# Optimization experiments

Hardware: AMD Instinct MI355X
Metric: run time of the kernel (lower is better)

## Reference

```python
import jax, jax.numpy as jnp
import numpy as np
from jax import lax

B_SZ, L, D_MODEL = 2, 2048, 1024
D_INNER, D_STATE, D_CONV, DT_RANK = 2048, 16, 4, 64


def setup_inputs() -> dict:
    key = jax.random.key(0)
    ks = jax.random.split(key, 9)
    s = 0.02
    x = jax.random.normal(ks[0], (B_SZ, L, D_MODEL), dtype=jnp.float32)
    W_in = jax.random.normal(ks[1], (D_MODEL, 2 * D_INNER), dtype=jnp.float32) * s
    conv_w = jax.random.normal(ks[2], (D_INNER, D_CONV), dtype=jnp.float32) * s
    conv_b = jax.random.normal(ks[3], (D_INNER,), dtype=jnp.float32) * s
    W_x = jax.random.normal(ks[4], (D_INNER, DT_RANK + 2 * D_STATE), dtype=jnp.float32) * s
    W_dt = jax.random.normal(ks[5], (DT_RANK, D_INNER), dtype=jnp.float32) * s
    b_dt = jax.random.normal(ks[6], (D_INNER,), dtype=jnp.float32) * s
    A_log = jnp.log(jnp.broadcast_to(jnp.arange(1, D_STATE + 1, dtype=jnp.float32), (D_INNER, D_STATE)))
    D = jnp.ones((D_INNER,), dtype=jnp.float32)
    W_out = jax.random.normal(ks[7], (D_INNER, D_MODEL), dtype=jnp.float32) * s
    return {"x": x, "W_in": W_in, "conv_w": conv_w, "conv_b": conv_b,
            "W_x": W_x, "W_dt": W_dt, "b_dt": b_dt, "A_log": A_log, "D": D, "W_out": W_out}


def _silu(v):
    return v * jax.nn.sigmoid(v)


def _mamba_fwd(x, W_in, conv_w, conv_b, W_x, W_dt, b_dt, A_log, D, W_out):
    b, l, _ = x.shape
    xz = x @ W_in                                  # [b,l,2*d_inner]
    xs, res = jnp.split(xz, 2, axis=-1)
    # causal depthwise conv1d (torch pads d_conv-1 both sides then truncates to l -> left pad only)
    xc = xs.transpose(0, 2, 1)                     # [b,d_inner,l]
    xc = lax.conv_general_dilated(
        xc, conv_w[:, None, :], window_strides=(1,),
        padding=[(D_CONV - 1, 0)], feature_group_count=D_INNER,
        dimension_numbers=("NCH", "OIH", "NCH")) + conv_b[None, :, None]
    u = _silu(xc.transpose(0, 2, 1))               # [b,l,d_inner]
    # projections for delta, B, C
    x_dbl = u @ W_x                                # [b,l,dt_rank+2n]
    dt, Bm, Cm = jnp.split(x_dbl, [DT_RANK, DT_RANK + D_STATE], axis=-1)
    delta = jax.nn.softplus(dt @ W_dt + b_dt)      # [b,l,d_inner]
    A = -jnp.exp(A_log)                            # [d_inner,n]

    def step(h, inp):
        d_t, B_t, C_t, u_t = inp                   # [b,d_in],[b,n],[b,n],[b,d_in]
        dA = jnp.exp(d_t[:, :, None] * A)          # [b,d_in,n]
        h = dA * h + d_t[:, :, None] * B_t[:, None, :] * u_t[:, :, None]
        y = jnp.einsum("bdn,bn->bd", h, C_t)
        return h, y

    h0 = jnp.zeros((b, D_INNER, D_STATE), dtype=u.dtype)
    _, ys = lax.scan(step, h0, (delta.transpose(1, 0, 2), Bm.transpose(1, 0, 2),
                                Cm.transpose(1, 0, 2), u.transpose(1, 0, 2)))
    y = ys.transpose(1, 0, 2) + u * D              # [b,l,d_inner]
    y = y * _silu(res)
    return y @ W_out                               # [b,l,d_model]


def reference(x, W_in, conv_w, conv_b, W_x, W_dt, b_dt, A_log, D, W_out):
    return _mamba_fwd(x, W_in, conv_w, conv_b, W_x, W_dt, b_dt, A_log, D, W_out)
```

## Files before the change

### kernel.cpp

```cpp
#include <hip/hip_runtime.h>
#include <hip/hip_bf16.h>
#include <math.h>

#define B_SZ    2
#define LSEQ    2048
#define DMODEL  1024
#define DINNER  2048
#define DSTATE  16
#define DCONV   4
#define DTRANK  64

#define NCHUNK  64
#define CLEN    (LSEQ / NCHUNK)

#define KSPLIT  16
#define NX      96

typedef unsigned short u16;
typedef __bf16 bf16x8 __attribute__((ext_vector_type(8)));
typedef float  f32x4  __attribute__((ext_vector_type(4)));

static __device__ __forceinline__ float sigmoidf_(float x) {
    return 1.0f / (1.0f + __expf(-x));
}
static __device__ __forceinline__ u16 f2b(float f) {
    unsigned int u = __float_as_uint(f);
    u = (u + 0x7fffu + ((u >> 16) & 1u)) >> 16;
    return (u16)u;
}
static __device__ __forceinline__ float b2f(u16 v) {
    return __uint_as_float(((unsigned int)v) << 16);
}

__global__ __launch_bounds__(256) void cast_bf16(
    const float* __restrict__ in, u16* __restrict__ out, int n8)
{
    const int i = blockIdx.x * 256 + threadIdx.x;
    if (i >= n8) return;
    const float4* p = reinterpret_cast<const float4*>(in + (size_t)i * 8);
    float4 v0 = p[0], v1 = p[1];
    union { u16 u[8]; uint4 q; } r;
    r.u[0] = f2b(v0.x); r.u[1] = f2b(v0.y); r.u[2] = f2b(v0.z); r.u[3] = f2b(v0.w);
    r.u[4] = f2b(v1.x); r.u[5] = f2b(v1.y); r.u[6] = f2b(v1.z); r.u[7] = f2b(v1.w);
    reinterpret_cast<uint4*>(out)[i] = r.q;
}

__global__ __launch_bounds__(256) void castT_bf16(
    const float* __restrict__ in, u16* __restrict__ out, int R, int C)
{
    __shared__ float t[32][33];
    const int r0 = blockIdx.y * 32, c0 = blockIdx.x * 32;
    const int tr = threadIdx.x >> 3;
    const int tc4 = (threadIdx.x & 7) * 4;
    const float4 v = *reinterpret_cast<const float4*>(in + (size_t)(r0 + tr) * C + c0 + tc4);
    t[tr][tc4 + 0] = v.x; t[tr][tc4 + 1] = v.y; t[tr][tc4 + 2] = v.z; t[tr][tc4 + 3] = v.w;
    __syncthreads();
    union { u16 u[4]; uint2 q; } r;
    #pragma unroll
    for (int j = 0; j < 4; j++) r.u[j] = f2b(t[tc4 + j][tr]);
    *reinterpret_cast<uint2*>(out + (size_t)(c0 + tr) * R + r0 + tc4) = r.q;
}

__global__ __launch_bounds__(256) void gemm_bf16_split(
    const u16* __restrict__ A, const u16* __restrict__ Bt,
    u16* __restrict__ xs_bf, u16* __restrict__ zs_bf, int K)
{
    __shared__ u16 As[128 * 32];
    __shared__ u16 Bs[128 * 32];
    const int tid  = threadIdx.x;
    const int lane = tid & 63;
    const int wave = tid >> 6;
    const int wr = wave >> 1, wc = wave & 1;
    const int bm = blockIdx.y * 128, bn = blockIdx.x * 128;
    const int lhi = lane >> 4;
    const int llo = lane & 15;

    f32x4 acc[4][4] = {};

    for (int k0 = 0; k0 < K; k0 += 32) {
        #pragma unroll
        for (int c = 0; c < 2; ++c) {
            const int s   = c * 256 + wave * 64 + lane;
            const int row = s >> 2, seg = s & 3;
            const u16* ga = A  + (size_t)(bm + row) * K + k0 + seg * 8;
            const u16* gb = Bt + (size_t)(bn + row) * K + k0 + seg * 8;
            __builtin_amdgcn_global_load_lds(
                (const __attribute__((address_space(1))) void*)ga,
                (__attribute__((address_space(3))) void*)(As + (size_t)(c * 256 + wave * 64) * 8),
                16, 0, 0);
            __builtin_amdgcn_global_load_lds(
                (const __attribute__((address_space(1))) void*)gb,
                (__attribute__((address_space(3))) void*)(Bs + (size_t)(c * 256 + wave * 64) * 8),
                16, 0, 0);
        }
        __syncthreads();

        bf16x8 af[4], bfr[4];
        #pragma unroll
        for (int m = 0; m < 4; ++m)
            af[m] = *reinterpret_cast<const bf16x8*>(&As[(wr * 64 + m * 16 + llo) * 32 + lhi * 8]);
        #pragma unroll
        for (int n = 0; n < 4; ++n)
            bfr[n] = *reinterpret_cast<const bf16x8*>(&Bs[(wc * 64 + n * 16 + llo) * 32 + lhi * 8]);
        #pragma unroll
        for (int m = 0; m < 4; ++m)
            #pragma unroll
            for (int n = 0; n < 4; ++n)
                acc[m][n] = __builtin_amdgcn_mfma_f32_16x16x32_bf16(af[m], bfr[n], acc[m][n], 0, 0, 0);
        __syncthreads();
    }

    #pragma unroll
    for (int m = 0; m < 4; ++m) {
        const int row0 = bm + wr * 64 + m * 16 + lhi * 4;
        #pragma unroll
        for (int n = 0; n < 4; ++n) {
            const int col = bn + wc * 64 + n * 16 + llo;
            #pragma unroll
            for (int j = 0; j < 4; ++j) {
                float v = acc[m][n][j];
                if (col < DINNER) {
                    xs_bf[(size_t)(row0 + j) * DINNER + col] = f2b(v);
                } else {
                    v = v * sigmoidf_(v);
                    zs_bf[(size_t)(row0 + j) * DINNER + (col - DINNER)] = f2b(v);
                }
            }
        }
    }
}

__global__ __launch_bounds__(256) void gemm_bf16_tn(
    const u16* __restrict__ A, const u16* __restrict__ Bt,
    float* __restrict__ C, int M, int N, int K, int ldc)
{
    __shared__ u16 As[128 * 32];
    __shared__ u16 Bs[128 * 32];
    const int tid  = threadIdx.x;
    const int lane = tid & 63;
    const int wave = tid >> 6;
    const int wr = wave >> 1, wc = wave & 1;
    const int bm = blockIdx.y * 128, bn = blockIdx.x * 128;
    const int lhi = lane >> 4;
    const int llo = lane & 15;

    f32x4 acc[4][4] = {};

    for (int k0 = 0; k0 < K; k0 += 32) {
        #pragma unroll
        for (int c = 0; c < 2; ++c) {
            const int s   = c * 256 + wave * 64 + lane;
            const int row = s >> 2, seg = s & 3;
            const u16* ga = A  + (size_t)(bm + row) * K + k0 + seg * 8;
            const u16* gb = Bt + (size_t)(bn + row) * K + k0 + seg * 8;
            __builtin_amdgcn_global_load_lds(
                (const __attribute__((address_space(1))) void*)ga,
                (__attribute__((address_space(3))) void*)(As + (size_t)(c * 256 + wave * 64) * 8),
                16, 0, 0);
            __builtin_amdgcn_global_load_lds(
                (const __attribute__((address_space(1))) void*)gb,
                (__attribute__((address_space(3))) void*)(Bs + (size_t)(c * 256 + wave * 64) * 8),
                16, 0, 0);
        }
        __syncthreads();

        bf16x8 af[4], bfr[4];
        #pragma unroll
        for (int m = 0; m < 4; ++m)
            af[m] = *reinterpret_cast<const bf16x8*>(&As[(wr * 64 + m * 16 + llo) * 32 + lhi * 8]);
        #pragma unroll
        for (int n = 0; n < 4; ++n)
            bfr[n] = *reinterpret_cast<const bf16x8*>(&Bs[(wc * 64 + n * 16 + llo) * 32 + lhi * 8]);
        #pragma unroll
        for (int m = 0; m < 4; ++m)
            #pragma unroll
            for (int n = 0; n < 4; ++n)
                acc[m][n] = __builtin_amdgcn_mfma_f32_16x16x32_bf16(af[m], bfr[n], acc[m][n], 0, 0, 0);
        __syncthreads();
    }

    #pragma unroll
    for (int m = 0; m < 4; ++m) {
        const int row0 = bm + wr * 64 + m * 16 + lhi * 4;
        #pragma unroll
        for (int n = 0; n < 4; ++n) {
            const int col = bn + wc * 64 + n * 16 + llo;
            #pragma unroll
            for (int j = 0; j < 4; ++j)
                C[(size_t)(row0 + j) * ldc + col] = acc[m][n][j];
        }
    }
}

__global__ __launch_bounds__(256) void conv_silu_bf(
    const u16* __restrict__ xs, const float* __restrict__ conv_w,
    const float* __restrict__ conv_b, u16* __restrict__ u)
{
    const int g  = blockIdx.x * 256 + threadIdx.x;
    const int d8 = (g & 255) * 8;
    const int bl = g >> 8;
    const int l  = bl & (LSEQ - 1);

    float4 wv[8];
    #pragma unroll
    for (int j = 0; j < 8; j++)
        wv[j] = *reinterpret_cast<const float4*>(conv_w + (size_t)(d8 + j) * DCONV);

    float acc[8];
    #pragma unroll
    for (int j = 0; j < 8; j++) acc[j] = conv_b[d8 + j];

    #pragma unroll
    for (int k = 0; k < DCONV; k++) {
        const int l2 = l - (DCONV - 1) + k;
        if (l2 < 0) continue;
        const uint4 q = *reinterpret_cast<const uint4*>(
            xs + (size_t)(bl - (DCONV - 1) + k) * DINNER + d8);
        const u16* e = reinterpret_cast<const u16*>(&q);
        #pragma unroll
        for (int j = 0; j < 8; j++) {
            const float w = (k == 0) ? wv[j].x : (k == 1) ? wv[j].y : (k == 2) ? wv[j].z : wv[j].w;
            acc[j] = fmaf(b2f(e[j]), w, acc[j]);
        }
    }
    union { u16 u[8]; uint4 q; } r;
    #pragma unroll
    for (int j = 0; j < 8; j++) {
        const float v = acc[j];
        r.u[j] = f2b(v * sigmoidf_(v));
    }
    *reinterpret_cast<uint4*>(u + (size_t)bl * DINNER + d8) = r.q;
}

__global__ __launch_bounds__(256) void gemm3_splitk(
    const u16* __restrict__ ubf, const float* __restrict__ Wx,
    float* __restrict__ partial)
{
    __shared__ float us[64][65];
    __shared__ float wsm[64][96];

    const int tid = threadIdx.x;
    const int r0 = blockIdx.x * 64;
    const int k0 = blockIdx.y * (DINNER / KSPLIT);

    const int orow = tid >> 2;
    const int oc0  = (tid & 3) * 24;

    float acc[24];
    #pragma unroll
    for (int j = 0; j < 24; j++) acc[j] = 0.f;

    for (int ks = 0; ks < DINNER / KSPLIT; ks += 64) {
        {
            const int row = tid >> 2;
            const int c16 = (tid & 3) << 4;
            const uint4* src = reinterpret_cast<const uint4*>(
                ubf + (size_t)(r0 + row) * DINNER + k0 + ks + c16);
            const uint4 q0 = src[0], q1 = src[1];
            const u16* e0 = reinterpret_cast<const u16*>(&q0);
            const u16* e1 = reinterpret_cast<const u16*>(&q1);
            #pragma unroll
            for (int j = 0; j < 8; j++) us[row][c16 + j]     = b2f(e0[j]);
            #pragma unroll
            for (int j = 0; j < 8; j++) us[row][c16 + 8 + j] = b2f(e1[j]);
        }
        #pragma unroll
        for (int j = 0; j < 6; j++) {
            const int fid = tid + j * 256;
            const int kr  = fid / 24;
            const int c4  = (fid % 24) * 4;
            *reinterpret_cast<float4*>(&wsm[kr][c4]) =
                *reinterpret_cast<const float4*>(Wx + (size_t)(k0 + ks + kr) * NX + c4);
        }
        __syncthreads();

        for (int kk = 0; kk < 64; ++kk) {
            const float uv = us[orow][kk];
            #pragma unroll
            for (int j = 0; j < 24; j++)
                acc[j] = fmaf(uv, wsm[kk][oc0 + j], acc[j]);
        }
        __syncthreads();
    }

    float* pp = partial + ((size_t)blockIdx.y * (B_SZ * LSEQ) + r0 + orow) * NX + oc0;
    #pragma unroll
    for (int j = 0; j < 24; j += 4)
        *reinterpret_cast<float4*>(pp + j) = make_float4(acc[j], acc[j+1], acc[j+2], acc[j+3]);
}

__global__ __launch_bounds__(256) void gemm3_reduce(
    const float* __restrict__ partial, float* __restrict__ xdbl)
{
    const int i = blockIdx.x * 256 + threadIdx.x;
    if (i >= B_SZ * LSEQ * NX / 4) return;
    float4 s = make_float4(0.f, 0.f, 0.f, 0.f);
    #pragma unroll
    for (int p = 0; p < KSPLIT; p++) {
        const float4 v = reinterpret_cast<const float4*>(
            partial + (size_t)p * (B_SZ * LSEQ) * NX)[i];
        s.x += v.x; s.y += v.y; s.z += v.z; s.w += v.w;
    }
    reinterpret_cast<float4*>(xdbl)[i] = s;
}

__global__ __launch_bounds__(256) void scan_phase1(
    const u16* __restrict__ ubf, const float* __restrict__ xdbl,
    const float* __restrict__ Wdt, const float* __restrict__ bdt,
    const float* __restrict__ A_log,
    float* __restrict__ hend, float* __restrict__ Sd, u16* __restrict__ delta_bf)
{
    const int idx = blockIdx.x * 256 + threadIdx.x;
    const int d = idx & (DINNER - 1);
    const int c = (idx >> 11) & (NCHUNK - 1);
    const int b = idx >> 17;

    float w[DTRANK];
    #pragma unroll
    for (int k = 0; k < DTRANK; k++) w[k] = Wdt[(size_t)k * DINNER + d];
    const float bb = bdt[d];

    float a[DSTATE];
    #pragma unroll
    for (int n = 0; n < DSTATE; n++) a[n] = -__expf(A_log[d * DSTATE + n]);

    float h[DSTATE];
    #pragma unroll
    for (int n = 0; n < DSTATE; n++) h[n] = 0.f;
    float sd = 0.f;

    const int l0 = b * LSEQ + c * CLEN;
    for (int i = 0; i < CLEN; ++i) {
        const size_t r = (size_t)(l0 + i);
        const float* xr = xdbl + r * NX;

        float t = bb;
        #pragma unroll
        for (int k = 0; k < DTRANK; k += 4) {
            const float4 v = *reinterpret_cast<const float4*>(xr + k);
            t = fmaf(w[k],     v.x, t);
            t = fmaf(w[k + 1], v.y, t);
            t = fmaf(w[k + 2], v.z, t);
            t = fmaf(w[k + 3], v.w, t);
        }
        const float dv = (t > 20.f) ? t : log1pf(__expf(t));
        sd += dv;
        delta_bf[r * DINNER + d] = f2b(dv);

        const float uv = b2f(ubf[r * DINNER + d]);

        float Bv[DSTATE];
        {
            const float4* bp = reinterpret_cast<const float4*>(xr + DTRANK);
            float4 q;
            q = bp[0]; Bv[0]=q.x;  Bv[1]=q.y;  Bv[2]=q.z;  Bv[3]=q.w;
            q = bp[1]; Bv[4]=q.x;  Bv[5]=q.y;  Bv[6]=q.z;  Bv[7]=q.w;
            q = bp[2]; Bv[8]=q.x;  Bv[9]=q.y;  Bv[10]=q.z; Bv[11]=q.w;
            q = bp[3]; Bv[12]=q.x; Bv[13]=q.y; Bv[14]=q.z; Bv[15]=q.w;
        }
        const float du = dv * uv;
        #pragma unroll
        for (int n = 0; n < DSTATE; n++)
            h[n] = fmaf(__expf(dv * a[n]), h[n], du * Bv[n]);
    }

    float* hp = hend + ((size_t)(b * DINNER + d) * NCHUNK + c) * DSTATE;
    #pragma unroll
    for (int n = 0; n < DSTATE; n += 4)
        *reinterpret_cast<float4*>(hp + n) = make_float4(h[n], h[n+1], h[n+2], h[n+3]);
    Sd[(size_t)(b * DINNER + d) * NCHUNK + c] = sd;
}

__global__ __launch_bounds__(256) void scan_phase2(
    float* __restrict__ hend, const float* __restrict__ Sd,
    const float* __restrict__ A_log)
{
    const int idx = blockIdx.x * 256 + threadIdx.x;
    if (idx >= B_SZ * DINNER * DSTATE) return;
    const int n = idx & (DSTATE - 1);
    const int d = (idx >> 4) & (DINNER - 1);
    const int b = idx >> 15;

    const float an = -__expf(A_log[d * DSTATE + n]);
    const size_t base = (size_t)(b * DINNER + d) * NCHUNK;
    float carry = 0.f;
    for (int c = 0; c < NCHUNK; ++c) {
        const float P = __expf(an * Sd[base + c]);
        const size_t off = (base + c) * DSTATE + n;
        const float tmp = hend[off];
        hend[off] = carry;
        carry = fmaf(P, carry, tmp);
    }
}

__global__ __launch_bounds__(256) void scan_phase3(
    const u16* __restrict__ delta_bf, const u16* __restrict__ ubf,
    const u16* __restrict__ zs_bf, const float* __restrict__ xdbl,
    const float* __restrict__ A_log, const float* __restrict__ Dp,
    const float* __restrict__ hin, u16* __restrict__ ybf)
{
    const int idx = blockIdx.x * 256 + threadIdx.x;
    const int d = idx & (DINNER - 1);
    const int c = (idx >> 11) & (NCHUNK - 1);
    const int b = idx >> 17;

    float a[DSTATE];
    #pragma unroll
    for (int n = 0; n < DSTATE; n++) a[n] = -__expf(A_log[d * DSTATE + n]);
    const float Dd = Dp[d];

    float h[DSTATE];
    {
        const float* hp = hin + ((size_t)(b * DINNER + d) * NCHUNK + c) * DSTATE;
        #pragma unroll
        for (int n = 0; n < DSTATE; n += 4) {
            const float4 t = *reinterpret_cast<const float4*>(hp + n);
            h[n] = t.x; h[n+1] = t.y; h[n+2] = t.z; h[n+3] = t.w;
        }
    }

    const int l0 = b * LSEQ + c * CLEN;
    for (int i = 0; i < CLEN; ++i) {
        const size_t r = (size_t)(l0 + i);
        const float dv = b2f(delta_bf[r * DINNER + d]);
        const float uv = b2f(ubf[r * DINNER + d]);

        const float4* bp = reinterpret_cast<const float4*>(xdbl + r * NX + DTRANK);
        float Bv[DSTATE], Cv[DSTATE];
        {
            float4 t;
            t = bp[0]; Bv[0]=t.x;  Bv[1]=t.y;  Bv[2]=t.z;  Bv[3]=t.w;
            t = bp[1]; Bv[4]=t.x;  Bv[5]=t.y;  Bv[6]=t.z;  Bv[7]=t.w;
            t = bp[2]; Bv[8]=t.x;  Bv[9]=t.y;  Bv[10]=t.z; Bv[11]=t.w;
            t = bp[3]; Bv[12]=t.x; Bv[13]=t.y; Bv[14]=t.z; Bv[15]=t.w;
            t = bp[4]; Cv[0]=t.x;  Cv[1]=t.y;  Cv[2]=t.z;  Cv[3]=t.w;
            t = bp[5]; Cv[4]=t.x;  Cv[5]=t.y;  Cv[6]=t.z;  Cv[7]=t.w;
            t = bp[6]; Cv[8]=t.x;  Cv[9]=t.y;  Cv[10]=t.z; Cv[11]=t.w;
            t = bp[7]; Cv[12]=t.x; Cv[13]=t.y; Cv[14]=t.z; Cv[15]=t.w;
        }

        const float du = dv * uv;
        float yv = 0.f;
        #pragma unroll
        for (int n = 0; n < DSTATE; n++) {
            h[n] = fmaf(__expf(dv * a[n]), h[n], du * Bv[n]);
            yv = fmaf(h[n], Cv[n], yv);
        }
        yv = fmaf(uv, Dd, yv);

        const float g = b2f(zs_bf[r * DINNER + d]);
        ybf[r * DINNER + d] = f2b(yv * g);
    }
}

extern "C" void kernel_launch(void* const* d_in, const int* in_sizes, int n_in,
                              void* d_out, int out_size, void* d_ws, size_t ws_size,
                              hipStream_t stream) {
    const float* x      = (const float*)d_in[0];
    const float* W_in   = (const float*)d_in[1];
    const float* conv_w = (const float*)d_in[2];
    const float* conv_b = (const float*)d_in[3];
    const float* W_x    = (const float*)d_in[4];
    const float* W_dt   = (const float*)d_in[5];
    const float* b_dt   = (const float*)d_in[6];
    const float* A_log  = (const float*)d_in[7];
    const float* Dp     = (const float*)d_in[8];
    const float* W_out  = (const float*)d_in[9];
    float* out = (float*)d_out;

    const int M = B_SZ * LSEQ;

    float* ws    = (float*)d_ws;
    float* xdbl  = ws;
    float* hend  = xdbl + (size_t)M * NX;
    float* Sd    = hend + (size_t)B_SZ * DINNER * NCHUNK * DSTATE;
    float* part  = Sd   + (size_t)B_SZ * DINNER * NCHUNK;
    u16*   xs_bf = (u16*)(part + (size_t)KSPLIT * M * NX);
    u16*   zs_bf = xs_bf + (size_t)M * DINNER;
    u16*   u_bf  = zs_bf + (size_t)M * DINNER;
    u16*   dl_bf = u_bf  + (size_t)M * DINNER;
    u16*   xbf   = dl_bf + (size_t)M * DINNER;
    u16*   WinT  = xbf   + (size_t)M * DMODEL;
    u16*   WoutT = WinT  + (size_t)M * DMODEL;
    u16*   ybf   = xbf;

    dim3 blk(256);

    cast_bf16<<<dim3((M * DMODEL / 8) / 256), blk, 0, stream>>>(x, xbf, M * DMODEL / 8);
    castT_bf16<<<dim3((2 * DINNER) / 32, DMODEL / 32), blk, 0, stream>>>(
        W_in, WinT, DMODEL, 2 * DINNER);

    gemm_bf16_split<<<dim3((2 * DINNER) / 128, M / 128), blk, 0, stream>>>(
        xbf, WinT, xs_bf, zs_bf, DMODEL);

    conv_silu_bf<<<dim3((M * DINNER / 8) / 256), blk, 0, stream>>>(
        xs_bf, conv_w, conv_b, u_bf);

    gemm3_splitk<<<dim3(M / 64, KSPLIT), blk, 0, stream>>>(u_bf, W_x, part);
    gemm3_reduce<<<dim3((M * NX / 4 + 255) / 256), blk, 0, stream>>>(part, xdbl);

    scan_phase1<<<dim3((B_SZ * DINNER * NCHUNK) / 256), blk, 0, stream>>>(
        u_bf, xdbl, W_dt, b_dt, A_log, hend, Sd, dl_bf);
    scan_phase2<<<dim3((B_SZ * DINNER * DSTATE) / 256), blk, 0, stream>>>(
        hend, Sd, A_log);
    scan_phase3<<<dim3((B_SZ * DINNER * NCHUNK) / 256), blk, 0, stream>>>(
        dl_bf, u_bf, zs_bf, xdbl, A_log, Dp, hend, ybf);

    castT_bf16<<<dim3(DMODEL / 32, DINNER / 32), blk, 0, stream>>>(
        W_out, WoutT, DINNER, DMODEL);

    gemm_bf16_tn<<<dim3(DMODEL / 128, M / 128), blk, 0, stream>>>(
        ybf, WoutT, out, M, DMODEL, DINNER, DMODEL);
}
```

Measured before the change: 441.2 us.

## Move delta projection to MFMA GEMM with softplus epilogue and swizzle LDS

The per-thread scalar dt@W_dt dot product (64 FMAs per step, run inside scan_phase1) is replaced by a separate bf16 MFMA GEMM with a fused bias+softplus epilogue that writes delta as bf16. The reduce kernel now also emits a bf16 copy of the dt columns. The shared MFMA GEMM template also gains an XOR swizzle on LDS segment placement to reduce bank conflicts. This adds two launches and a bf16 rounding of dt inputs, in exchange for removing the 64-register weight load and the FMA loop from the scan.

```diff
diff --git a/kernel.cpp b/kernel.cpp
--- a/kernel.cpp
+++ b/kernel.cpp
@@ -61,9 +61,11 @@
     *reinterpret_cast<uint2*>(out + (size_t)(c0 + tr) * R + r0 + tc4) = r.q;
 }
 
-__global__ __launch_bounds__(256) void gemm_bf16_split(
+template<int EPI>
+__global__ __launch_bounds__(256) void gemm_mfma(
     const u16* __restrict__ A, const u16* __restrict__ Bt,
-    u16* __restrict__ xs_bf, u16* __restrict__ zs_bf, int K)
+    float* __restrict__ Cf, u16* __restrict__ o0, u16* __restrict__ o1,
+    const float* __restrict__ bias, int M, int N, int K, int ldc)
 {
     __shared__ u16 As[128 * 32];
     __shared__ u16 Bs[128 * 32];
@@ -77,13 +79,16 @@
 
     f32x4 acc[4][4] = {};
 
+    const int rs = (lhi ^ ((llo >> 1) & 3)) * 8;
+
     for (int k0 = 0; k0 < K; k0 += 32) {
         #pragma unroll
         for (int c = 0; c < 2; ++c) {
             const int s   = c * 256 + wave * 64 + lane;
             const int row = s >> 2, seg = s & 3;
-            const u16* ga = A  + (size_t)(bm + row) * K + k0 + seg * 8;
-            const u16* gb = Bt + (size_t)(bn + row) * K + k0 + seg * 8;
+            const int sseg = seg ^ ((row >> 1) & 3);
+            const u16* ga = A  + (size_t)(bm + row) * K + k0 + sseg * 8;
+            const u16* gb = Bt + (size_t)(bn + row) * K + k0 + sseg * 8;
             __builtin_amdgcn_global_load_lds(
                 (const __attribute__((address_space(1))) void*)ga,
                 (__attribute__((address_space(3))) void*)(As + (size_t)(c * 256 + wave * 64) * 8),
@@ -98,10 +103,10 @@
         bf16x8 af[4], bfr[4];
         #pragma unroll
         for (int m = 0; m < 4; ++m)
-            af[m] = *reinterpret_cast<const bf16x8*>(&As[(wr * 64 + m * 16 + llo) * 32 + lhi * 8]);
+            af[m] = *reinterpret_cast<const bf16x8*>(&As[(wr * 64 + m * 16 + llo) * 32 + rs]);
         #pragma unroll
         for (int n = 0; n < 4; ++n)
-            bfr[n] = *reinterpret_cast<const bf16x8*>(&Bs[(wc * 64 + n * 16 + llo) * 32 + lhi * 8]);
+            bfr[n] = *reinterpret_cast<const bf16x8*>(&Bs[(wc * 64 + n * 16 + llo) * 32 + rs]);
         #pragma unroll
         for (int m = 0; m < 4; ++m)
             #pragma unroll
@@ -119,75 +124,21 @@
             #pragma unroll
             for (int j = 0; j < 4; ++j) {
                 float v = acc[m][n][j];
-                if (col < DINNER) {
-                    xs_bf[(size_t)(row0 + j) * DINNER + col] = f2b(v);
+                if (EPI == 0) {
+                    Cf[(size_t)(row0 + j) * ldc + col] = v;
+                } else if (EPI == 1) {
+                    if (col < DINNER) {
+                        o0[(size_t)(row0 + j) * DINNER + col] = f2b(v);
+                    } else {
+                        v = v * sigmoidf_(v);
+                        o1[(size_t)(row0 + j) * DINNER + (col - DINNER)] = f2b(v);
+                    }
                 } else {
-                    v = v * sigmoidf_(v);
-                    zs_bf[(size_t)(row0 + j) * DINNER + (col - DINNER)] = f2b(v);
+                    v += bias[col];
+                    v = (v > 20.f) ? v : log1pf(__expf(v));
+                    o0[(size_t)(row0 + j) * ldc + col] = f2b(v);
                 }
             }
-        }
-    }
-}
-
-__global__ __launch_bounds__(256) void gemm_bf16_tn(
-    const u16* __restrict__ A, const u16* __restrict__ Bt,
-    float* __restrict__ C, int M, int N, int K, int ldc)
-{
-    __shared__ u16 As[128 * 32];
-    __shared__ u16 Bs[128 * 32];
-    const int tid  = threadIdx.x;
-    const int lane = tid & 63;
-    const int wave = tid >> 6;
-    const int wr = wave >> 1, wc = wave & 1;
-    const int bm = blockIdx.y * 128, bn = blockIdx.x * 128;
-    const int lhi = lane >> 4;
-    const int llo = lane & 15;
-
-    f32x4 acc[4][4] = {};
-
-    for (int k0 = 0; k0 < K; k0 += 32) {
-        #pragma unroll
-        for (int c = 0; c < 2; ++c) {
-            const int s   = c * 256 + wave * 64 + lane;
-            const int row = s >> 2, seg = s & 3;
-            const u16* ga = A  + (size_t)(bm + row) * K + k0 + seg * 8;
-            const u16* gb = Bt + (size_t)(bn + row) * K + k0 + seg * 8;
-            __builtin_amdgcn_global_load_lds(
-                (const __attribute__((address_space(1))) void*)ga,
-                (__attribute__((address_space(3))) void*)(As + (size_t)(c * 256 + wave * 64) * 8),
-                16, 0, 0);
-            __builtin_amdgcn_global_load_lds(
-                (const __attribute__((address_space(1))) void*)gb,
-                (__attribute__((address_space(3))) void*)(Bs + (size_t)(c * 256 + wave * 64) * 8),
-                16, 0, 0);
-        }
-        __syncthreads();
-
-        bf16x8 af[4], bfr[4];
-        #pragma unroll
-        for (int m = 0; m < 4; ++m)
-            af[m] = *reinterpret_cast<const bf16x8*>(&As[(wr * 64 + m * 16 + llo) * 32 + lhi * 8]);
-        #pragma unroll
-        for (int n = 0; n < 4; ++n)
-            bfr[n] = *reinterpret_cast<const bf16x8*>(&Bs[(wc * 64 + n * 16 + llo) * 32 + lhi * 8]);
-        #pragma unroll
-        for (int m = 0; m < 4; ++m)
-            #pragma unroll
-            for (int n = 0; n < 4; ++n)
-                acc[m][n] = __builtin_amdgcn_mfma_f32_16x16x32_bf16(af[m], bfr[n], acc[m][n], 0, 0, 0);
-        __syncthreads();
-    }
-
-    #pragma unroll
-    for (int m = 0; m < 4; ++m) {
-        const int row0 = bm + wr * 64 + m * 16 + lhi * 4;
-        #pragma unroll
-        for (int n = 0; n < 4; ++n) {
-            const int col = bn + wc * 64 + n * 16 + llo;
-            #pragma unroll
-            for (int j = 0; j < 4; ++j)
-                C[(size_t)(row0 + j) * ldc + col] = acc[m][n][j];
         }
     }
 }
@@ -290,7 +241,8 @@
 }
 
 __global__ __launch_bounds__(256) void gemm3_reduce(
-    const float* __restrict__ partial, float* __restrict__ xdbl)
+    const float* __restrict__ partial, float* __restrict__ xdbl,
+    u16* __restrict__ x64bf)
 {
     const int i = blockIdx.x * 256 + threadIdx.x;
     if (i >= B_SZ * LSEQ * NX / 4) return;
@@ -302,24 +254,26 @@
         s.x += v.x; s.y += v.y; s.z += v.z; s.w += v.w;
     }
     reinterpret_cast<float4*>(xdbl)[i] = s;
+
+    const int col4 = (i % 24) * 4;
+    if (col4 < DTRANK) {
+        const int row = i / 24;
+        union { u16 u[4]; uint2 q; } r;
+        r.u[0] = f2b(s.x); r.u[1] = f2b(s.y); r.u[2] = f2b(s.z); r.u[3] = f2b(s.w);
+        *reinterpret_cast<uint2*>(x64bf + (size_t)row * DTRANK + col4) = r.q;
+    }
 }
 
 __global__ __launch_bounds__(256) void scan_phase1(
-    const u16* __restrict__ ubf, const float* __restrict__ xdbl,
-    const float* __restrict__ Wdt, const float* __restrict__ bdt,
-    const float* __restrict__ A_log,
-    float* __restrict__ hend, float* __restrict__ Sd, u16* __restrict__ delta_bf)
+    const u16* __restrict__ dl_bf, const u16* __restrict__ ubf,
+    const float* __restrict__ xdbl, const float* __restrict__ A_log,
+    float* __restrict__ hend, float* __restrict__ Sd)
 {
     const int idx = blockIdx.x * 256 + threadIdx.x;
     const int d = idx & (DINNER - 1);
     const int c = (idx >> 11) & (NCHUNK - 1);
     const int b = idx >> 17;
 
-    float w[DTRANK];
-    #pragma unroll
-    for (int k = 0; k < DTRANK; k++) w[k] = Wdt[(size_t)k * DINNER + d];
-    const float bb = bdt[d];
-
     float a[DSTATE];
     #pragma unroll
     for (int n = 0; n < DSTATE; n++) a[n] = -__expf(A_log[d * DSTATE + n]);
@@ -332,26 +286,12 @@
     const int l0 = b * LSEQ + c * CLEN;
     for (int i = 0; i < CLEN; ++i) {
         const size_t r = (size_t)(l0 + i);
-        const float* xr = xdbl + r * NX;
-
-        float t = bb;
-        #pragma unroll
-        for (int k = 0; k < DTRANK; k += 4) {
-            const float4 v = *reinterpret_cast<const float4*>(xr + k);
-            t = fmaf(w[k],     v.x, t);
-            t = fmaf(w[k + 1], v.y, t);
-            t = fmaf(w[k + 2], v.z, t);
-            t = fmaf(w[k + 3], v.w, t);
-        }
-        const float dv = (t > 20.f) ? t : log1pf(__expf(t));
+        const float dv = b2f(dl_bf[r * DINNER + d]);
+        const float uv = b2f(ubf[r * DINNER + d]);
         sd += dv;
-        delta_bf[r * DINNER + d] = f2b(dv);
-
-        const float uv = b2f(ubf[r * DINNER + d]);
-
         float Bv[DSTATE];
         {
-            const float4* bp = reinterpret_cast<const float4*>(xr + DTRANK);
+            const float4* bp = reinterpret_cast<const float4*>(xdbl + r * NX + DTRANK);
             float4 q;
             q = bp[0]; Bv[0]=q.x;  Bv[1]=q.y;  Bv[2]=q.z;  Bv[3]=q.w;
             q = bp[1]; Bv[4]=q.x;  Bv[5]=q.y;  Bv[6]=q.z;  Bv[7]=q.w;
@@ -394,7 +334,7 @@
 }
 
 __global__ __launch_bounds__(256) void scan_phase3(
-    const u16* __restrict__ delta_bf, const u16* __restrict__ ubf,
+    const u16* __restrict__ dl_bf, const u16* __restrict__ ubf,
     const u16* __restrict__ zs_bf, const float* __restrict__ xdbl,
     const float* __restrict__ A_log, const float* __restrict__ Dp,
     const float* __restrict__ hin, u16* __restrict__ ybf)
@@ -422,7 +362,7 @@
     const int l0 = b * LSEQ + c * CLEN;
     for (int i = 0; i < CLEN; ++i) {
         const size_t r = (size_t)(l0 + i);
-        const float dv = b2f(delta_bf[r * DINNER + d]);
+        const float dv = b2f(dl_bf[r * DINNER + d]);
         const float uv = b2f(ubf[r * DINNER + d]);
 
         const float4* bp = reinterpret_cast<const float4*>(xdbl + r * NX + DTRANK);
@@ -470,19 +410,21 @@
 
     const int M = B_SZ * LSEQ;
 
-    float* ws    = (float*)d_ws;
-    float* xdbl  = ws;
-    float* hend  = xdbl + (size_t)M * NX;
-    float* Sd    = hend + (size_t)B_SZ * DINNER * NCHUNK * DSTATE;
-    float* part  = Sd   + (size_t)B_SZ * DINNER * NCHUNK;
-    u16*   xs_bf = (u16*)(part + (size_t)KSPLIT * M * NX);
-    u16*   zs_bf = xs_bf + (size_t)M * DINNER;
-    u16*   u_bf  = zs_bf + (size_t)M * DINNER;
-    u16*   dl_bf = u_bf  + (size_t)M * DINNER;
-    u16*   xbf   = dl_bf + (size_t)M * DINNER;
-    u16*   WinT  = xbf   + (size_t)M * DMODEL;
-    u16*   WoutT = WinT  + (size_t)M * DMODEL;
-    u16*   ybf   = xbf;
+    float* ws     = (float*)d_ws;
+    float* xdbl   = ws;
+    float* hend   = xdbl + (size_t)M * NX;
+    float* Sd     = hend + (size_t)B_SZ * DINNER * NCHUNK * DSTATE;
+    float* part   = Sd   + (size_t)B_SZ * DINNER * NCHUNK;
+    u16*   xs_bf  = (u16*)(part + (size_t)KSPLIT * M * NX);
+    u16*   zs_bf  = xs_bf + (size_t)M * DINNER;
+    u16*   u_bf   = zs_bf + (size_t)M * DINNER;
+    u16*   dl_bf  = u_bf  + (size_t)M * DINNER;
+    u16*   xbf    = dl_bf + (size_t)M * DINNER;
+    u16*   WinT   = xbf   + (size_t)M * DMODEL;
+    u16*   WoutT  = WinT  + (size_t)M * DMODEL;
+    u16*   x64bf  = WoutT + (size_t)DMODEL * DINNER;
+    u16*   WdtT   = x64bf + (size_t)M * DTRANK;
+    u16*   ybf    = xbf;
 
     dim3 blk(256);
 
@@ -490,17 +432,22 @@
     castT_bf16<<<dim3((2 * DINNER) / 32, DMODEL / 32), blk, 0, stream>>>(
         W_in, WinT, DMODEL, 2 * DINNER);
 
-    gemm_bf16_split<<<dim3((2 * DINNER) / 128, M / 128), blk, 0, stream>>>(
-        xbf, WinT, xs_bf, zs_bf, DMODEL);
+    gemm_mfma<1><<<dim3((2 * DINNER) / 128, M / 128), blk, 0, stream>>>(
+        xbf, WinT, nullptr, xs_bf, zs_bf, nullptr, M, 2 * DINNER, DMODEL, 0);
 
     conv_silu_bf<<<dim3((M * DINNER / 8) / 256), blk, 0, stream>>>(
         xs_bf, conv_w, conv_b, u_bf);
 
     gemm3_splitk<<<dim3(M / 64, KSPLIT), blk, 0, stream>>>(u_bf, W_x, part);
-    gemm3_reduce<<<dim3((M * NX / 4 + 255) / 256), blk, 0, stream>>>(part, xdbl);
+    gemm3_reduce<<<dim3((M * NX / 4 + 255) / 256), blk, 0, stream>>>(part, xdbl, x64bf);
+
+    castT_bf16<<<dim3(DINNER / 32, DTRANK / 32), blk, 0, stream>>>(
+        W_dt, WdtT, DTRANK, DINNER);
+    gemm_mfma<2><<<dim3(DINNER / 128, M / 128), blk, 0, stream>>>(
+        x64bf, WdtT, nullptr, dl_bf, nullptr, b_dt, M, DINNER, DTRANK, DINNER);
 
     scan_phase1<<<dim3((B_SZ * DINNER * NCHUNK) / 256), blk, 0, stream>>>(
-        u_bf, xdbl, W_dt, b_dt, A_log, hend, Sd, dl_bf);
+        dl_bf, u_bf, xdbl, A_log, hend, Sd);
     scan_phase2<<<dim3((B_SZ * DINNER * DSTATE) / 256), blk, 0, stream>>>(
         hend, Sd, A_log);
     scan_phase3<<<dim3((B_SZ * DINNER * NCHUNK) / 256), blk, 0, stream>>>(
@@ -509,6 +456,6 @@
     castT_bf16<<<dim3(DMODEL / 32, DINNER / 32), blk, 0, stream>>>(
         W_out, WoutT, DINNER, DMODEL);
 
-    gemm_bf16_tn<<<dim3(DMODEL / 128, M / 128), blk, 0, stream>>>(
-        ybf, WoutT, out, M, DMODEL, DINNER, DMODEL);
-}
+    gemm_mfma<0><<<dim3(DMODEL / 128, M / 128), blk, 0, stream>>>(
+        ybf, WoutT, out, nullptr, nullptr, nullptr, M, DMODEL, DINNER, DMODEL);
+}
```

Result: faster. 408.8 us (-7.3%).
